# Optimization experiments

Measured on AMD Instinct MI355X. Metric: run time of the kernel, lower is better.

The kernel has to match this reference:

```python
import jax, jax.numpy as jnp
import numpy as np
import math

N_HEAD = 16

def _rope_cos_sin(T, head_dim):
    # thetas[i] = 10000 ** (-2*(i-1)/dim) for i = 1..dim/2  ->  exponent -2*j/dim, j=0..dim/2-1
    j = jnp.arange(head_dim // 2, dtype=jnp.float32)
    theta = jnp.power(10000.0, -2.0 * j / head_dim)          # [d/2]
    t = jnp.arange(T, dtype=jnp.float32)                      # [T]
    ang = t[:, None] * theta[None, :]                         # [T, d/2]
    return jnp.cos(ang), jnp.sin(ang)

def _apply_rope(u, cos, sin):
    # u: [B,H,T,d]; interleaved complex rotation over pairs (u[...,2i], u[...,2i+1])
    B, H, T, d = u.shape
    u = u.reshape(B, H, T, d // 2, 2)
    u0, u1 = u[..., 0], u[..., 1]
    r0 = u0 * cos - u1 * sin
    r1 = u0 * sin + u1 * cos
    return jnp.stack([r0, r1], axis=-1).reshape(B, H, T, d)

def setup_inputs() -> dict:
    key = jax.random.key(0)
    ks = jax.random.split(key, 9)
    C = 1024
    s = 1.0 / math.sqrt(C)
    return {
        "x": jax.random.normal(ks[0], (4, 2048, C), dtype=jnp.float32),
        "wq": jax.random.normal(ks[1], (C, C), dtype=jnp.float32) * s,
        "bq": jax.random.normal(ks[2], (C,), dtype=jnp.float32) * s,
        "wk": jax.random.normal(ks[3], (C, C), dtype=jnp.float32) * s,
        "bk": jax.random.normal(ks[4], (C,), dtype=jnp.float32) * s,
        "wv": jax.random.normal(ks[5], (C, C), dtype=jnp.float32) * s,
        "bv": jax.random.normal(ks[6], (C,), dtype=jnp.float32) * s,
        "wp": jax.random.normal(ks[7], (C, C), dtype=jnp.float32) * s,
        "bp": jax.random.normal(ks[8], (C,), dtype=jnp.float32) * s,
    }

def reference(x, wq, bq, wk, bk, wv, bv, wp, bp):
    B, T, C = x.shape
    H = N_HEAD
    d = C // H
    def proj(w, b):
        # nn.Linear: x @ w.T + b, then split heads -> [B,H,T,d]
        return (jnp.einsum('btc,oc->bto', x, w) + b).reshape(B, T, H, d).transpose(0, 2, 1, 3)
    q, k, v = proj(wq, bq), proj(wk, bk), proj(wv, bv)
    cos, sin = _rope_cos_sin(T, d)
    q = _apply_rope(q, cos, sin)
    k = _apply_rope(k, cos, sin)
    att = jnp.einsum('bhqd,bhkd->bhqk', q, k) * (1.0 / math.sqrt(d))  # [B,H,T,T]
    causal = jnp.tril(jnp.ones((T, T), dtype=bool))
    att = jnp.where(causal, att, jnp.finfo(att.dtype).min)
    att = jax.nn.softmax(att, axis=-1)
    y = jnp.einsum('bhqk,bhkd->bhqd', att, v)                         # [B,H,T,d]
    y = y.transpose(0, 2, 1, 3).reshape(B, T, C)
    return jnp.einsum('btc,oc->bto', y, wp) + bp
```

## Files before the change

kernel.cpp:

```cpp
#include <hip/hip_runtime.h>

typedef __attribute__((ext_vector_type(8))) __bf16 bf16x8;
typedef __attribute__((ext_vector_type(4))) float f32x4;
typedef __attribute__((ext_vector_type(16))) float f32x16;
typedef unsigned short u16;

#define TSEQ   2048
#define NB     4
#define NHEAD  16
#define HDIM   64
#define CMODEL 1024
#define MTOK   (NB*TSEQ)

__device__ __forceinline__ u16 f2bf(float x){
  unsigned u = __float_as_uint(x);
  u += 0x7fffu + ((u >> 16) & 1u);
  return (u16)(u >> 16);
}

__device__ __forceinline__ unsigned cvtpk(float lo, float hi){
  unsigned r;
  asm("v_cvt_pk_bf16_f32 %0, %1, %2" : "=v"(r) : "v"(lo), "v"(hi));
  return r;
}
__device__ __forceinline__ void plswap(unsigned &a, unsigned &b){
  asm volatile("v_permlane32_swap_b32 %0, %1" : "+v"(a), "+v"(b));
}

__device__ __forceinline__ void async16(const void* g, const u16* lds_base){
  __builtin_amdgcn_global_load_lds(
      (const __attribute__((address_space(1))) unsigned*)(uintptr_t)g,
      (__attribute__((address_space(3))) unsigned*)(unsigned)(uintptr_t)lds_base,
      16, 0, 0);
}

__global__ void cast_bf16_kernel(const float* __restrict__ src, u16* __restrict__ dst, int n4){
  int i = blockIdx.x * blockDim.x + threadIdx.x;
  int stride = gridDim.x * blockDim.x;
  for (; i < n4; i += stride){
    float4 v = ((const float4*)src)[i];
    ((ushort4*)dst)[i] = make_ushort4(f2bf(v.x), f2bf(v.y), f2bf(v.z), f2bf(v.w));
  }
}

__global__ void cast4_bf16_kernel(const float* __restrict__ s0, const float* __restrict__ s1,
                                  const float* __restrict__ s2, const float* __restrict__ s3,
                                  u16* __restrict__ d0, u16* __restrict__ d1,
                                  u16* __restrict__ d2, u16* __restrict__ d3, int n4){
  int which = blockIdx.y;
  const float* s = (which==0)?s0:(which==1)?s1:(which==2)?s2:s3;
  u16* d        = (which==0)?d0:(which==1)?d1:(which==2)?d2:d3;
  int i = blockIdx.x * blockDim.x + threadIdx.x;
  int stride = gridDim.x * blockDim.x;
  for (; i < n4; i += stride){
    float4 v = ((const float4*)s)[i];
    ((ushort4*)d)[i] = make_ushort4(f2bf(v.x), f2bf(v.y), f2bf(v.z), f2bf(v.w));
  }
}

__global__ void rope_table_kernel(float2* __restrict__ rope){
  int i = blockIdx.x * blockDim.x + threadIdx.x;
  if (i >= TSEQ * (HDIM/2)) return;
  int t = i >> 5, j = i & 31;
  float theta = exp2f(-(float)j * (13.287712379549449f / 32.f));
  float ang = (float)t * theta;
  rope[i] = make_float2(cosf(ang), sinf(ang));
}

__device__ __forceinline__ void gemm128_mainloop(
    const u16* __restrict__ A, const u16* __restrict__ B,
    int m0, int n0, int K, u16* sA, u16* sB, f32x4 acc[4][4])
{
  const int tid = threadIdx.x;
  const int w = tid >> 6, lane = tid & 63;
  const int ln = lane & 15, g = lane >> 4;
  const int wm = w >> 1, wn = w & 1;

  const f32x4 zero = {0.f, 0.f, 0.f, 0.f};
#pragma unroll
  for (int mt = 0; mt < 4; ++mt)
#pragma unroll
    for (int nt = 0; nt < 4; ++nt) acc[mt][nt] = zero;

  for (int k0 = 0; k0 < K; k0 += 64){
    __syncthreads();
#pragma unroll
    for (int i = 0; i < 4; ++i){
      int c = i*256 + tid;
      int r = c >> 3, sl = c & 7;
      int ks = sl ^ (r & 7);
      async16(A + (size_t)(m0 + r)*K + k0 + ks*8, sA + (size_t)(i*256 + w*64)*8);
      async16(B + (size_t)(n0 + r)*K + k0 + ks*8, sB + (size_t)(i*256 + w*64)*8);
    }
    __syncthreads();

#pragma unroll
    for (int kk = 0; kk < 2; ++kk){
      bf16x8 af[4], bfr[4];
#pragma unroll
      for (int mt = 0; mt < 4; ++mt){
        int row = wm*64 + mt*16 + ln;
        int sl = (kk*4 + g) ^ (row & 7);
        af[mt] = *(const bf16x8*)&sA[row*64 + sl*8];
      }
#pragma unroll
      for (int nt = 0; nt < 4; ++nt){
        int row = wn*64 + nt*16 + ln;
        int sl = (kk*4 + g) ^ (row & 7);
        bfr[nt] = *(const bf16x8*)&sB[row*64 + sl*8];
      }
      __builtin_amdgcn_s_setprio(1);
#pragma unroll
      for (int mt = 0; mt < 4; ++mt)
#pragma unroll
        for (int nt = 0; nt < 4; ++nt)
          acc[mt][nt] = __builtin_amdgcn_mfma_f32_16x16x32_bf16(af[mt], bfr[nt], acc[mt][nt], 0, 0, 0);
      __builtin_amdgcn_s_setprio(0);
    }
  }
}

#define SCQ 0.18033688011112042f

__global__ __launch_bounds__(256) void gemm_qkv_kernel(
    const u16* __restrict__ xb,
    const u16* __restrict__ wqb, const u16* __restrict__ wkb, const u16* __restrict__ wvb,
    const float* __restrict__ bq, const float* __restrict__ bk, const float* __restrict__ bv,
    const float2* __restrict__ rope,
    u16* __restrict__ Qh, u16* __restrict__ Kh, u16* __restrict__ Vt)
{
  __shared__ u16 sA[128*64];
  __shared__ u16 sB[128*64];
  const int z = blockIdx.z;
  const u16*  W    = (z == 0) ? wqb : (z == 1) ? wkb : wvb;
  const float* bias = (z == 0) ? bq  : (z == 1) ? bk  : bv;
  const int m0 = blockIdx.y * 128, n0 = blockIdx.x * 128;

  f32x4 acc[4][4];
  gemm128_mainloop(xb, W, m0, n0, CMODEL, sA, sB, acc);

  const int tid = threadIdx.x, w = tid >> 6, lane = tid & 63;
  const int ln = lane & 15, g = lane >> 4;
  const int wm = w >> 1, wn = w & 1;

#pragma unroll
  for (int mt = 0; mt < 4; ++mt){
#pragma unroll
    for (int nt = 0; nt < 4; ++nt){
      int o  = n0 + wn*64 + nt*16 + ln;
      float bb = bias[o];
      int h  = o >> 6;
      int dd = o & 63;
      if (z < 2){
        int j = dd >> 1;
        u16* dst = (z == 0) ? Qh : Kh;
        float qs = (z == 0) ? SCQ : 1.0f;
#pragma unroll
        for (int rr = 0; rr < 4; ++rr){
          int t  = m0 + wm*64 + mt*16 + g*4 + rr;
          int b  = t >> 11, tt = t & (TSEQ-1);
          float v  = acc[mt][nt][rr] + bb;
          float pv = __shfl_xor(v, 1);
          float2 cs = rope[tt*32 + j];
          float out = ((o & 1) == 0) ? (v*cs.x - pv*cs.y) : (pv*cs.y + v*cs.x);
          dst[(size_t)((b*NHEAD + h)*TSEQ + tt)*HDIM + dd] = f2bf(out * qs);
        }
      } else {
        int t0 = m0 + wm*64 + mt*16 + g*4;
        int b  = t0 >> 11, tt0 = t0 & (TSEQ-1);
        u16 pk[4];
#pragma unroll
        for (int rr = 0; rr < 4; ++rr) pk[rr] = f2bf(acc[mt][nt][rr] + bb);
        *(ushort4*)&Vt[(size_t)((b*NHEAD + h)*HDIM + dd)*TSEQ + tt0] =
            make_ushort4(pk[0], pk[1], pk[2], pk[3]);
      }
    }
  }
}

__global__ __launch_bounds__(128) void attn_kernel(
    const u16* __restrict__ Qh, const u16* __restrict__ Kh,
    const u16* __restrict__ Vt, u16* __restrict__ yb)
{
  __shared__ u16 sK[2][64*64];
  __shared__ u16 sV[2][64*64];

  const int tid = threadIdx.x, w = tid >> 6, lane = tid & 63;
  const int ln = lane & 31, hi = lane >> 5;

  const int bid = blockIdx.x;
  const int t   = 31 - (bid >> 6);
  const int bh  = (bid & 7) * 8 + ((bid >> 3) & 7);
  const int b   = bh >> 4, h = bh & (NHEAD-1);

  const u16* Qbase = Qh + (size_t)bh * TSEQ * HDIM;
  const u16* Kbase = Kh + (size_t)bh * TSEQ * HDIM;
  const u16* Vbase = Vt + (size_t)bh * HDIM * TSEQ;

  const int r0 = t*64 + w*32;

  const int swz = ln & 7;
  const f32x16 zero16 = {0,0,0,0,0,0,0,0,0,0,0,0,0,0,0,0};

  const u16* kp[4]; const u16* vp[4]; unsigned dstc[4];
#pragma unroll
  for (int i = 0; i < 4; ++i){
    int c = i*128 + tid, r = c >> 3, pc = c & 7;
    kp[i]   = Kbase + (size_t)r*HDIM + ((pc ^ (r&7))<<3);
    vp[i]   = Vbase + (size_t)r*TSEQ + ((pc ^ (r&7))<<3);
    dstc[i] = (unsigned)(i*128 + w*64)*8;
  }

  unsigned offd[4];
#pragma unroll
  for (int d = 0; d < 4; ++d) offd[d] = ((unsigned)((2*d + hi) ^ swz)) * 8;
  const unsigned rowl = (unsigned)ln * 64;
  const unsigned rowh = rowl + 32*64;

  bf16x8 qf[4];
#pragma unroll
  for (int ds = 0; ds < 4; ++ds)
    qf[ds] = *(const bf16x8*)&Qbase[(size_t)(r0 + ln)*HDIM + ds*16 + hi*8];

  f32x16 yacc0 = zero16, yacc1 = zero16;
  float m2 = -1e30f, lp = 0.f;

  int buf = 0;
#pragma unroll
  for (int i = 0; i < 4; ++i){
    async16(kp[i], sK[0] + dstc[i]);
    async16(vp[i], sV[0] + dstc[i]);
  }

#pragma unroll 1
  for (int jt = 0; jt <= t; ++jt){
    __syncthreads();
    if (jt < t){
      const size_t ko = (size_t)(jt+1) * (64*HDIM);
      const size_t vo = (size_t)(jt+1) * 64;
      u16* sKb = sK[buf^1]; u16* sVb = sV[buf^1];
#pragma unroll
      for (int i = 0; i < 4; ++i){
        async16(kp[i] + ko, sKb + dstc[i]);
        async16(vp[i] + vo, sVb + dstc[i]);
      }
    }

    const u16* sKb = sK[buf];
    const u16* sVb = sV[buf];
    const bool full1 = (jt < t) || w;

    f32x16 p0 = zero16, p1 = zero16;
    __builtin_amdgcn_s_setprio(1);
#pragma unroll
    for (int ds = 0; ds < 4; ++ds){
      bf16x8 k0 = *(const bf16x8*)&sKb[rowl + offd[ds]];
      p0 = __builtin_amdgcn_mfma_f32_32x32x16_bf16(k0, qf[ds], p0, 0, 0, 0);
    }
    if (full1){
#pragma unroll
      for (int ds = 0; ds < 4; ++ds){
        bf16x8 k1 = *(const bf16x8*)&sKb[rowh + offd[ds]];
        p1 = __builtin_amdgcn_mfma_f32_32x32x16_bf16(k1, qf[ds], p1, 0, 0, 0);
      }
    }
    __builtin_amdgcn_s_setprio(0);

    if (jt == t){
#pragma unroll
      for (int r = 0; r < 16; ++r){
        int k0r = (r&3) + 8*(r>>2) + 4*hi;
        bool cut = k0r > ln;
        if (!w){ if (cut) p0[r] = -1e30f; }
        else   { if (cut) p1[r] = -1e30f; }
      }
    }

    float lm = p0[0];
#pragma unroll
    for (int r = 1; r < 16; ++r) lm = fmaxf(lm, p0[r]);
    if (full1){
#pragma unroll
      for (int r = 0; r < 16; ++r) lm = fmaxf(lm, p1[r]);
    }

    if (__any(lm - m2 > 8.0f)){
      float lmp = __shfl_xor(lm, 32);
      float mn  = fmaxf(m2, fmaxf(lm, lmp));
      float scl = exp2f(m2 - mn);
      m2 = mn;
      lp *= scl;
#pragma unroll
      for (int r = 0; r < 16; ++r){
        float sr = __shfl(scl, (r&3) + 8*(r>>2) + 4*hi);
        yacc0[r] *= sr; yacc1[r] *= sr;
      }
    }

    float ts = 0.f;
#pragma unroll
    for (int r = 0; r < 16; ++r){ p0[r] = exp2f(p0[r] - m2); ts += p0[r]; }
    if (full1){
#pragma unroll
      for (int r = 0; r < 16; ++r){ p1[r] = exp2f(p1[r] - m2); ts += p1[r]; }
    }
    lp += ts;

    bf16x8 pa[4];
    {
      union { unsigned u[4]; bf16x8 v; } f0, f1;
      unsigned A0 = cvtpk(p0[0], p0[1]),  B0 = cvtpk(p0[2], p0[3]);
      unsigned A1 = cvtpk(p0[4], p0[5]),  B1 = cvtpk(p0[6], p0[7]);
      plswap(A0, A1); plswap(B0, B1);
      f0.u[0]=A0; f0.u[1]=B0; f0.u[2]=A1; f0.u[3]=B1;  pa[0]=f0.v;
      unsigned A2 = cvtpk(p0[8], p0[9]),  B2 = cvtpk(p0[10], p0[11]);
      unsigned A3 = cvtpk(p0[12], p0[13]),B3 = cvtpk(p0[14], p0[15]);
      plswap(A2, A3); plswap(B2, B3);
      f1.u[0]=A2; f1.u[1]=B2; f1.u[2]=A3; f1.u[3]=B3;  pa[1]=f1.v;
    }
    if (full1){
      union { unsigned u[4]; bf16x8 v; } f2, f3;
      unsigned A4 = cvtpk(p1[0], p1[1]),  B4 = cvtpk(p1[2], p1[3]);
      unsigned A5 = cvtpk(p1[4], p1[5]),  B5 = cvtpk(p1[6], p1[7]);
      plswap(A4, A5); plswap(B4, B5);
      f2.u[0]=A4; f2.u[1]=B4; f2.u[2]=A5; f2.u[3]=B5;  pa[2]=f2.v;
      unsigned A6 = cvtpk(p1[8], p1[9]),  B6 = cvtpk(p1[10], p1[11]);
      unsigned A7 = cvtpk(p1[12], p1[13]),B7 = cvtpk(p1[14], p1[15]);
      plswap(A6, A7); plswap(B6, B7);
      f3.u[0]=A6; f3.u[1]=B6; f3.u[2]=A7; f3.u[3]=B7;  pa[3]=f3.v;
    }

    __builtin_amdgcn_s_setprio(1);
#pragma unroll
    for (int st = 0; st < 2; ++st){
      bf16x8 v0 = *(const bf16x8*)&sVb[rowl + offd[st]];
      bf16x8 v1 = *(const bf16x8*)&sVb[rowh + offd[st]];
      yacc0 = __builtin_amdgcn_mfma_f32_32x32x16_bf16(pa[st], v0, yacc0, 0, 0, 0);
      yacc1 = __builtin_amdgcn_mfma_f32_32x32x16_bf16(pa[st], v1, yacc1, 0, 0, 0);
    }
    if (full1){
#pragma unroll
      for (int st = 2; st < 4; ++st){
        bf16x8 v0 = *(const bf16x8*)&sVb[rowl + offd[st]];
        bf16x8 v1 = *(const bf16x8*)&sVb[rowh + offd[st]];
        yacc0 = __builtin_amdgcn_mfma_f32_32x32x16_bf16(pa[st], v0, yacc0, 0, 0, 0);
        yacc1 = __builtin_amdgcn_mfma_f32_32x32x16_bf16(pa[st], v1, yacc1, 0, 0, 0);
      }
    }
    __builtin_amdgcn_s_setprio(0);

    buf ^= 1;
  }

  float lpf = lp + __shfl_xor(lp, 32);
  float inv = 1.0f / lpf;
#pragma unroll
  for (int r = 0; r < 16; ++r){
    int q = (r&3) + 8*(r>>2) + 4*hi;
    float ir = __shfl(inv, q);
    int tt = r0 + q;
    size_t rowoff = (size_t)(b*TSEQ + tt)*CMODEL + h*HDIM;
    yb[rowoff + ln]      = f2bf(yacc0[r] * ir);
    yb[rowoff + 32 + ln] = f2bf(yacc1[r] * ir);
  }
}

__global__ __launch_bounds__(256) void gemm_proj_kernel(
    const u16* __restrict__ yb, const u16* __restrict__ wpb,
    const float* __restrict__ bp, float* __restrict__ out)
{
  __shared__ u16 sA[128*64];
  __shared__ u16 sB[128*64];
  const int m0 = blockIdx.y * 128, n0 = blockIdx.x * 128;
  f32x4 acc[4][4];
  gemm128_mainloop(yb, wpb, m0, n0, CMODEL, sA, sB, acc);

  const int tid = threadIdx.x, w = tid >> 6, lane = tid & 63;
  const int ln = lane & 15, g = lane >> 4;
  const int wm = w >> 1, wn = w & 1;
#pragma unroll
  for (int mt = 0; mt < 4; ++mt)
#pragma unroll
    for (int nt = 0; nt < 4; ++nt){
      int o = n0 + wn*64 + nt*16 + ln;
      float bb = bp[o];
#pragma unroll
      for (int rr = 0; rr < 4; ++rr){
        int t = m0 + wm*64 + mt*16 + g*4 + rr;
        out[(size_t)t*CMODEL + o] = acc[mt][nt][rr] + bb;
      }
    }
}

extern "C" void kernel_launch(void* const* d_in, const int* in_sizes, int n_in,
                              void* d_out, int out_size, void* d_ws, size_t ws_size,
                              hipStream_t stream)
{
  const float* x  = (const float*)d_in[0];
  const float* wq = (const float*)d_in[1];
  const float* bq = (const float*)d_in[2];
  const float* wk = (const float*)d_in[3];
  const float* bk = (const float*)d_in[4];
  const float* wv = (const float*)d_in[5];
  const float* bv = (const float*)d_in[6];
  const float* wp = (const float*)d_in[7];
  const float* bp = (const float*)d_in[8];

  char* ws = (char*)d_ws;
  u16*    xb   = (u16*)   (ws + 0);
  u16*    wqb  = (u16*)   (ws + 16777216);
  u16*    wkb  = (u16*)   (ws + 18874368);
  u16*    wvb  = (u16*)   (ws + 20971520);
  u16*    wpb  = (u16*)   (ws + 23068672);
  float2* rope = (float2*)(ws + 25165824);
  u16*    Qh   = (u16*)   (ws + 25690112);
  u16*    Kh   = (u16*)   (ws + 42467328);
  u16*    Vt   = (u16*)   (ws + 59244544);
  u16*    yb   = (u16*)   (ws + 76021760);

  cast_bf16_kernel<<<2048, 256, 0, stream>>>(x,  xb,  MTOK*CMODEL/4);
  cast4_bf16_kernel<<<dim3(256, 4), 256, 0, stream>>>(wq, wk, wv, wp, wqb, wkb, wvb, wpb,
                                                      CMODEL*CMODEL/4);
  rope_table_kernel<<<(TSEQ*(HDIM/2) + 255)/256, 256, 0, stream>>>(rope);

  gemm_qkv_kernel<<<dim3(CMODEL/128, MTOK/128, 3), 256, 0, stream>>>(
      xb, wqb, wkb, wvb, bq, bk, bv, rope, Qh, Kh, Vt);

  attn_kernel<<<dim3(2048), 128, 0, stream>>>(Qh, Kh, Vt, yb);

  gemm_proj_kernel<<<dim3(CMODEL/128, MTOK/128), 256, 0, stream>>>(yb, wpb, bp, (float*)d_out);
}
```

Baseline: 216.8 us.

## Use triple-buffered 128x256 GEMM tiles with 8 waves and interleaved async loads

```diff
diff --git a/kernel.cpp b/kernel.cpp
--- a/kernel.cpp
+++ b/kernel.cpp
@@ -67,81 +67,179 @@
   rope[i] = make_float2(cosf(ang), sinf(ang));
 }
 
-__device__ __forceinline__ void gemm128_mainloop(
+#define AREG 8192
+#define BREG 16384
+
+__device__ __forceinline__ void gemm_tb3_mainloop(
     const u16* __restrict__ A, const u16* __restrict__ B,
-    int m0, int n0, int K, u16* sA, u16* sB, f32x4 acc[4][4])
+    int m0, int n0, u16* sAb, u16* sBb, f32x4 acc[4][4])
 {
   const int tid = threadIdx.x;
-  const int w = tid >> 6, lane = tid & 63;
+  const int lane = tid & 63, w = tid >> 6;
   const int ln = lane & 15, g = lane >> 4;
-  const int wm = w >> 1, wn = w & 1;
+  const int wm = w >> 2, wn = w & 3;
 
   const f32x4 zero = {0.f, 0.f, 0.f, 0.f};
 #pragma unroll
-  for (int mt = 0; mt < 4; ++mt)
-#pragma unroll
-    for (int nt = 0; nt < 4; ++nt) acc[mt][nt] = zero;
-
-  for (int k0 = 0; k0 < K; k0 += 64){
-    __syncthreads();
-#pragma unroll
-    for (int i = 0; i < 4; ++i){
-      int c = i*256 + tid;
-      int r = c >> 3, sl = c & 7;
-      int ks = sl ^ (r & 7);
-      async16(A + (size_t)(m0 + r)*K + k0 + ks*8, sA + (size_t)(i*256 + w*64)*8);
-      async16(B + (size_t)(n0 + r)*K + k0 + ks*8, sB + (size_t)(i*256 + w*64)*8);
-    }
-    __syncthreads();
-
-#pragma unroll
-    for (int kk = 0; kk < 2; ++kk){
-      bf16x8 af[4], bfr[4];
-#pragma unroll
-      for (int mt = 0; mt < 4; ++mt){
-        int row = wm*64 + mt*16 + ln;
-        int sl = (kk*4 + g) ^ (row & 7);
-        af[mt] = *(const bf16x8*)&sA[row*64 + sl*8];
-      }
-#pragma unroll
-      for (int nt = 0; nt < 4; ++nt){
-        int row = wn*64 + nt*16 + ln;
-        int sl = (kk*4 + g) ^ (row & 7);
-        bfr[nt] = *(const bf16x8*)&sB[row*64 + sl*8];
-      }
-      __builtin_amdgcn_s_setprio(1);
-#pragma unroll
-      for (int mt = 0; mt < 4; ++mt)
-#pragma unroll
-        for (int nt = 0; nt < 4; ++nt)
-          acc[mt][nt] = __builtin_amdgcn_mfma_f32_16x16x32_bf16(af[mt], bfr[nt], acc[mt][nt], 0, 0, 0);
-      __builtin_amdgcn_s_setprio(0);
-    }
+  for (int i = 0; i < 4; ++i)
+#pragma unroll
+    for (int nt = 0; nt < 4; ++nt) acc[i][nt] = zero;
+
+  const int cA0 = tid,       rA0 = cA0 >> 3;
+  const int cA1 = 512 + tid, rA1 = cA1 >> 3;
+  const u16* aS0 = A + (size_t)(m0 + rA0)*CMODEL + (((cA0 & 7) ^ (rA0 & 7)) << 3);
+  const u16* aS1 = A + (size_t)(m0 + rA1)*CMODEL + (((cA1 & 7) ^ (rA1 & 7)) << 3);
+  const unsigned dA0 = (unsigned)cA0 * 8, dA1 = (unsigned)cA1 * 8;
+  const u16* bS[4]; unsigned dB[4];
+#pragma unroll
+  for (int j = 0; j < 4; ++j){
+    int c = j*512 + tid, r = c >> 3;
+    bS[j] = B + (size_t)(n0 + r)*CMODEL + (((c & 7) ^ (r & 7)) << 3);
+    dB[j] = (unsigned)c * 8;
+  }
+
+  unsigned aoff[4][2], boff[4][2];
+#pragma unroll
+  for (int i = 0; i < 4; ++i){
+    int r = wm*64 + i*16 + ln;
+#pragma unroll
+    for (int kk = 0; kk < 2; ++kk)
+      aoff[i][kk] = (unsigned)(r*8 + ((kk*4 + g) ^ (r & 7))) * 8;
+  }
+#pragma unroll
+  for (int nt = 0; nt < 4; ++nt){
+    int r = wn*64 + nt*16 + ln;
+#pragma unroll
+    for (int kk = 0; kk < 2; ++kk)
+      boff[nt][kk] = (unsigned)(r*8 + ((kk*4 + g) ^ (r & 7))) * 8;
+  }
+
+  async16(aS0,       sAb + dA0);
+  async16(aS1,       sAb + dA1);
+  async16(bS[0],     sBb + dB[0]);
+  async16(bS[1],     sBb + dB[1]);
+  async16(bS[2],     sBb + dB[2]);
+  async16(bS[3],     sBb + dB[3]);
+  async16(aS0 + 64,  sAb + AREG + dA0);
+  async16(aS1 + 64,  sAb + AREG + dA1);
+  async16(bS[0] + 64, sBb + BREG + dB[0]);
+  async16(bS[1] + 64, sBb + BREG + dB[1]);
+  async16(bS[2] + 64, sBb + BREG + dB[2]);
+  async16(bS[3] + 64, sBb + BREG + dB[3]);
+  asm volatile("s_waitcnt vmcnt(6)" ::: "memory");
+  asm volatile("s_barrier" ::: "memory");
+
+#pragma unroll 1
+  for (int kt = 0; kt < 16; ++kt){
+    const int cb = kt % 3;
+    const int nb = (kt + 2) % 3;
+    const u16* Ab = sAb + cb*AREG;
+    const u16* Bb = sBb + cb*BREG;
+    u16* An = sAb + nb*AREG;
+    u16* Bn = sBb + nb*BREG;
+    const unsigned ko = (unsigned)(kt + 2) * 64u;
+    const bool st = (kt < 14);
+
+    bf16x8 a0, a1, a2, a3, b0, b1, b2, b3;
+
+    a0 = *(const bf16x8*)&Ab[aoff[0][0]];
+    a1 = *(const bf16x8*)&Ab[aoff[1][0]];
+    b0 = *(const bf16x8*)&Bb[boff[0][0]];
+    b1 = *(const bf16x8*)&Bb[boff[1][0]];
+    b2 = *(const bf16x8*)&Bb[boff[2][0]];
+    b3 = *(const bf16x8*)&Bb[boff[3][0]];
+    if (st){ async16(aS0 + ko, An + dA0); async16(aS1 + ko, An + dA1); }
+    asm volatile("s_barrier" ::: "memory");
+    __builtin_amdgcn_s_setprio(1);
+    acc[0][0] = __builtin_amdgcn_mfma_f32_16x16x32_bf16(a0, b0, acc[0][0], 0,0,0);
+    acc[0][1] = __builtin_amdgcn_mfma_f32_16x16x32_bf16(a0, b1, acc[0][1], 0,0,0);
+    acc[0][2] = __builtin_amdgcn_mfma_f32_16x16x32_bf16(a0, b2, acc[0][2], 0,0,0);
+    acc[0][3] = __builtin_amdgcn_mfma_f32_16x16x32_bf16(a0, b3, acc[0][3], 0,0,0);
+    acc[1][0] = __builtin_amdgcn_mfma_f32_16x16x32_bf16(a1, b0, acc[1][0], 0,0,0);
+    acc[1][1] = __builtin_amdgcn_mfma_f32_16x16x32_bf16(a1, b1, acc[1][1], 0,0,0);
+    acc[1][2] = __builtin_amdgcn_mfma_f32_16x16x32_bf16(a1, b2, acc[1][2], 0,0,0);
+    acc[1][3] = __builtin_amdgcn_mfma_f32_16x16x32_bf16(a1, b3, acc[1][3], 0,0,0);
+    __builtin_amdgcn_s_setprio(0);
+    asm volatile("s_barrier" ::: "memory");
+
+    a2 = *(const bf16x8*)&Ab[aoff[2][0]];
+    a3 = *(const bf16x8*)&Ab[aoff[3][0]];
+    if (st){ async16(bS[0] + ko, Bn + dB[0]); async16(bS[1] + ko, Bn + dB[1]); }
+    asm volatile("s_barrier" ::: "memory");
+    __builtin_amdgcn_s_setprio(1);
+    acc[2][0] = __builtin_amdgcn_mfma_f32_16x16x32_bf16(a2, b0, acc[2][0], 0,0,0);
+    acc[2][1] = __builtin_amdgcn_mfma_f32_16x16x32_bf16(a2, b1, acc[2][1], 0,0,0);
+    acc[2][2] = __builtin_amdgcn_mfma_f32_16x16x32_bf16(a2, b2, acc[2][2], 0,0,0);
+    acc[2][3] = __builtin_amdgcn_mfma_f32_16x16x32_bf16(a2, b3, acc[2][3], 0,0,0);
+    acc[3][0] = __builtin_amdgcn_mfma_f32_16x16x32_bf16(a3, b0, acc[3][0], 0,0,0);
+    acc[3][1] = __builtin_amdgcn_mfma_f32_16x16x32_bf16(a3, b1, acc[3][1], 0,0,0);
+    acc[3][2] = __builtin_amdgcn_mfma_f32_16x16x32_bf16(a3, b2, acc[3][2], 0,0,0);
+    acc[3][3] = __builtin_amdgcn_mfma_f32_16x16x32_bf16(a3, b3, acc[3][3], 0,0,0);
+    __builtin_amdgcn_s_setprio(0);
+    asm volatile("s_barrier" ::: "memory");
+
+    a0 = *(const bf16x8*)&Ab[aoff[0][1]];
+    a1 = *(const bf16x8*)&Ab[aoff[1][1]];
+    b0 = *(const bf16x8*)&Bb[boff[0][1]];
+    b1 = *(const bf16x8*)&Bb[boff[1][1]];
+    b2 = *(const bf16x8*)&Bb[boff[2][1]];
+    b3 = *(const bf16x8*)&Bb[boff[3][1]];
+    if (st) async16(bS[2] + ko, Bn + dB[2]);
+    asm volatile("s_barrier" ::: "memory");
+    __builtin_amdgcn_s_setprio(1);
+    acc[0][0] = __builtin_amdgcn_mfma_f32_16x16x32_bf16(a0, b0, acc[0][0], 0,0,0);
+    acc[0][1] = __builtin_amdgcn_mfma_f32_16x16x32_bf16(a0, b1, acc[0][1], 0,0,0);
+    acc[0][2] = __builtin_amdgcn_mfma_f32_16x16x32_bf16(a0, b2, acc[0][2], 0,0,0);
+    acc[0][3] = __builtin_amdgcn_mfma_f32_16x16x32_bf16(a0, b3, acc[0][3], 0,0,0);
+    acc[1][0] = __builtin_amdgcn_mfma_f32_16x16x32_bf16(a1, b0, acc[1][0], 0,0,0);
+    acc[1][1] = __builtin_amdgcn_mfma_f32_16x16x32_bf16(a1, b1, acc[1][1], 0,0,0);
+    acc[1][2] = __builtin_amdgcn_mfma_f32_16x16x32_bf16(a1, b2, acc[1][2], 0,0,0);
+    acc[1][3] = __builtin_amdgcn_mfma_f32_16x16x32_bf16(a1, b3, acc[1][3], 0,0,0);
+    __builtin_amdgcn_s_setprio(0);
+    asm volatile("s_barrier" ::: "memory");
+
+    a2 = *(const bf16x8*)&Ab[aoff[2][1]];
+    a3 = *(const bf16x8*)&Ab[aoff[3][1]];
+    if (st) async16(bS[3] + ko, Bn + dB[3]);
+    asm volatile("s_barrier" ::: "memory");
+    __builtin_amdgcn_s_setprio(1);
+    acc[2][0] = __builtin_amdgcn_mfma_f32_16x16x32_bf16(a2, b0, acc[2][0], 0,0,0);
+    acc[2][1] = __builtin_amdgcn_mfma_f32_16x16x32_bf16(a2, b1, acc[2][1], 0,0,0);
+    acc[2][2] = __builtin_amdgcn_mfma_f32_16x16x32_bf16(a2, b2, acc[2][2], 0,0,0);
+    acc[2][3] = __builtin_amdgcn_mfma_f32_16x16x32_bf16(a2, b3, acc[2][3], 0,0,0);
+    acc[3][0] = __builtin_amdgcn_mfma_f32_16x16x32_bf16(a3, b0, acc[3][0], 0,0,0);
+    acc[3][1] = __builtin_amdgcn_mfma_f32_16x16x32_bf16(a3, b1, acc[3][1], 0,0,0);
+    acc[3][2] = __builtin_amdgcn_mfma_f32_16x16x32_bf16(a3, b2, acc[3][2], 0,0,0);
+    acc[3][3] = __builtin_amdgcn_mfma_f32_16x16x32_bf16(a3, b3, acc[3][3], 0,0,0);
+    __builtin_amdgcn_s_setprio(0);
+    if (st) asm volatile("s_waitcnt vmcnt(6)" ::: "memory");
+    else    asm volatile("s_waitcnt vmcnt(0)" ::: "memory");
+    asm volatile("s_barrier" ::: "memory");
   }
 }
 
 #define SCQ 0.18033688011112042f
 
-__global__ __launch_bounds__(256) void gemm_qkv_kernel(
+__global__ __launch_bounds__(512, 1) void gemm_qkv_kernel(
     const u16* __restrict__ xb,
     const u16* __restrict__ wqb, const u16* __restrict__ wkb, const u16* __restrict__ wvb,
     const float* __restrict__ bq, const float* __restrict__ bk, const float* __restrict__ bv,
     const float2* __restrict__ rope,
     u16* __restrict__ Qh, u16* __restrict__ Kh, u16* __restrict__ Vt)
 {
-  __shared__ u16 sA[128*64];
-  __shared__ u16 sB[128*64];
+  __shared__ u16 sA[3*AREG];
+  __shared__ u16 sB[3*BREG];
   const int z = blockIdx.z;
   const u16*  W    = (z == 0) ? wqb : (z == 1) ? wkb : wvb;
   const float* bias = (z == 0) ? bq  : (z == 1) ? bk  : bv;
-  const int m0 = blockIdx.y * 128, n0 = blockIdx.x * 128;
+  const int m0 = blockIdx.y * 128, n0 = blockIdx.x * 256;
 
   f32x4 acc[4][4];
-  gemm128_mainloop(xb, W, m0, n0, CMODEL, sA, sB, acc);
+  gemm_tb3_mainloop(xb, W, m0, n0, sA, sB, acc);
 
   const int tid = threadIdx.x, w = tid >> 6, lane = tid & 63;
   const int ln = lane & 15, g = lane >> 4;
-  const int wm = w >> 1, wn = w & 1;
+  const int wm = w >> 2, wn = w & 3;
 
 #pragma unroll
   for (int mt = 0; mt < 4; ++mt){
@@ -365,19 +463,19 @@
   }
 }
 
-__global__ __launch_bounds__(256) void gemm_proj_kernel(
+__global__ __launch_bounds__(512, 1) void gemm_proj_kernel(
     const u16* __restrict__ yb, const u16* __restrict__ wpb,
     const float* __restrict__ bp, float* __restrict__ out)
 {
-  __shared__ u16 sA[128*64];
-  __shared__ u16 sB[128*64];
-  const int m0 = blockIdx.y * 128, n0 = blockIdx.x * 128;
+  __shared__ u16 sA[3*AREG];
+  __shared__ u16 sB[3*BREG];
+  const int m0 = blockIdx.y * 128, n0 = blockIdx.x * 256;
   f32x4 acc[4][4];
-  gemm128_mainloop(yb, wpb, m0, n0, CMODEL, sA, sB, acc);
+  gemm_tb3_mainloop(yb, wpb, m0, n0, sA, sB, acc);
 
   const int tid = threadIdx.x, w = tid >> 6, lane = tid & 63;
   const int ln = lane & 15, g = lane >> 4;
-  const int wm = w >> 1, wn = w & 1;
+  const int wm = w >> 2, wn = w & 3;
 #pragma unroll
   for (int mt = 0; mt < 4; ++mt)
 #pragma unroll
@@ -423,10 +521,10 @@
                                                       CMODEL*CMODEL/4);
   rope_table_kernel<<<(TSEQ*(HDIM/2) + 255)/256, 256, 0, stream>>>(rope);
 
-  gemm_qkv_kernel<<<dim3(CMODEL/128, MTOK/128, 3), 256, 0, stream>>>(
+  gemm_qkv_kernel<<<dim3(CMODEL/256, MTOK/128, 3), 512, 0, stream>>>(
       xb, wqb, wkb, wvb, bq, bk, bv, rope, Qh, Kh, Vt);
 
   attn_kernel<<<dim3(2048), 128, 0, stream>>>(Qh, Kh, Vt, yb);
 
-  gemm_proj_kernel<<<dim3(CMODEL/128, MTOK/128), 256, 0, stream>>>(yb, wpb, bp, (float*)d_out);
-}
+  gemm_proj_kernel<<<dim3(CMODEL/256, MTOK/128), 512, 0, stream>>>(yb, wpb, bp, (float*)d_out);
+}
```

Result: no change. 214.2 us (-1.2%).
